# Kernel optimization log

Measured on AMD Instinct MI355X. Metric: run time of the kernel, lower is better.

Reference implementation:

```python
import jax, jax.numpy as jnp
import numpy as np

N_NODES = 100000
NUM_FEAT = 64
NUM_CLASS = 40
N_EDGES = 1600000


def setup_inputs() -> dict:
    key = jax.random.key(0)
    k1, k2, k3, k4, k5 = jax.random.split(key, 5)
    x = jax.random.normal(k1, (N_NODES, NUM_FEAT), dtype=jnp.float32)
    index = jax.random.randint(k2, (2, N_EDGES), 0, N_NODES, dtype=jnp.int64)
    # SAGEConv params: lin_l applied to aggregated neighbors (has bias),
    # lin_r applied to root features (no bias) -- PyG convention.
    s = 1.0 / np.sqrt(NUM_FEAT)
    lin_l_w = jax.random.uniform(k3, (NUM_FEAT, NUM_CLASS), dtype=jnp.float32, minval=-s, maxval=s)
    lin_l_b = jnp.zeros((NUM_CLASS,), dtype=jnp.float32)
    lin_r_w = jax.random.uniform(k4, (NUM_FEAT, NUM_CLASS), dtype=jnp.float32, minval=-s, maxval=s)
    return {"x": x, "index": index, "lin_l_w": lin_l_w, "lin_l_b": lin_l_b, "lin_r_w": lin_r_w}


def reference(x, index, lin_l_w, lin_l_b, lin_r_w):
    src, dst = index[0], index[1]
    # Mean aggregation over incoming neighbors: messages flow src -> dst.
    msg = x[src]                                        # [E, F] gather
    agg_sum = jax.ops.segment_sum(msg, dst, num_segments=N_NODES)   # [N, F]
    deg = jax.ops.segment_sum(jnp.ones((index.shape[1],), dtype=x.dtype), dst,
                              num_segments=N_NODES)     # [N]
    agg = agg_sum / jnp.maximum(deg, 1.0)[:, None]      # mean, safe for isolated nodes
    out = agg @ lin_l_w + lin_l_b + x @ lin_r_w         # [N, C]
    return jax.nn.log_softmax(out, axis=1)
```

## Files before the change

### kernel.cpp

```cpp
#include <hip/hip_runtime.h>
#include <hip/hip_fp8.h>
#include <math.h>

constexpr int NODES = 100000;
constexpr int F = 64;
constexpr int C = 40;
constexpr int NPB   = 128;
constexpr int NB    = (NODES + NPB - 1) / NPB;
constexpr int NBPAD = 1024;
constexpr int BCAP  = 2816;
constexpr int TILE  = 4096;
constexpr int NTILES = NODES / 16;
constexpr int MBLK  = (NTILES + 3) / 4;

typedef __attribute__((ext_vector_type(8))) short short8;
typedef __attribute__((ext_vector_type(4))) float floatx4;
typedef __attribute__((ext_vector_type(2))) float floatx2;

__device__ inline unsigned bf16pack2(float a, float b) {
    unsigned ua = __builtin_bit_cast(unsigned, a);
    unsigned ub = __builtin_bit_cast(unsigned, b);
    ua += 0x7FFFu + ((ua >> 16) & 1u);
    ub += 0x7FFFu + ((ub >> 16) & 1u);
    return (ua >> 16) | (ub & 0xFFFF0000u);
}
__device__ inline unsigned short bf16of(float a) {
    unsigned ua = __builtin_bit_cast(unsigned, a);
    ua += 0x7FFFu + ((ua >> 16) & 1u);
    return (unsigned short)(ua >> 16);
}
__device__ inline float bf16tof(unsigned short u) {
    return __builtin_bit_cast(float, (unsigned)u << 16);
}
__device__ inline unsigned char fp8of(float f) {
    __hip_fp8_e4m3 q(f);
    return (unsigned char)q.__x;
}
template <int K>
__device__ inline float fp8byte(unsigned d) {
    __hip_fp8_e4m3 v;
    v.__x = (__hip_fp8_storage_t)((d >> (8 * K)) & 0xFFu);
    return (float)v;
}
template <int HI>
__device__ inline floatx2 fp8pk(unsigned d) {
#if __has_builtin(__builtin_amdgcn_cvt_pk_f32_fp8)
    return __builtin_amdgcn_cvt_pk_f32_fp8((int)d, HI != 0);
#else
    floatx2 r;
    r[0] = fp8byte<HI ? 2 : 0>(d);
    r[1] = fp8byte<HI ? 3 : 1>(d);
    return r;
#endif
}

__global__ __launch_bounds__(256)
void fused_A(const float* __restrict__ x,
             const float* __restrict__ wl,
             const float* __restrict__ bl,
             const float* __restrict__ wr,
             const int* __restrict__ src, const int* __restrict__ dst,
             int* __restrict__ gcursor, int* __restrict__ bbuf, int nedges,
             unsigned char* __restrict__ y8f, unsigned short* __restrict__ z8) {
    __shared__ union {
        struct { int lhist[NB]; int lcur[NB]; } bz;
        struct { unsigned sB[10 * 64 * 4]; float sbl[40]; } mf;
    } sh;

    int t = threadIdx.x;

    if (blockIdx.x < MBLK) {
        if (t < 40) sh.mf.sbl[t] = bl[t];
        for (int s = t; s < 640; s += 256) {
            int region = s >> 6;
            int l      = s & 63;
            int ct = region >> 1, ks = region & 1;
            int col = ct * 16 + (l & 15);
            int fb  = ks * 32 + ((l >> 4) << 3);
            const float* wsrc = (col < 40) ? (wl + col) : (wr + (col - 40));
            unsigned* dstp = &sh.mf.sB[s * 4];
#pragma unroll
            for (int p = 0; p < 4; ++p) {
                float a = wsrc[(fb + 2 * p) * 40];
                float b = wsrc[(fb + 2 * p + 1) * 40];
                dstp[p] = bf16pack2(a, b);
            }
        }
        __syncthreads();

        int lane = t & 63;
        int nt = blockIdx.x * 4 + (t >> 6);
        if (nt >= NTILES) return;

        union U { unsigned u[4]; short8 v; };
        short8 bf[5][2];
#pragma unroll
        for (int ct = 0; ct < 5; ++ct)
#pragma unroll
            for (int ks = 0; ks < 2; ++ks) {
                U tmp;
                const uint4* p =
                    (const uint4*)&sh.mf.sB[((ct * 2 + ks) * 64 + lane) * 4];
                uint4 q = *p;
                tmp.u[0] = q.x; tmp.u[1] = q.y; tmp.u[2] = q.z; tmp.u[3] = q.w;
                bf[ct][ks] = tmp.v;
            }

        floatx4 acc[5];
#pragma unroll
        for (int ct = 0; ct < 5; ++ct) {
            int col = ct * 16 + (lane & 15);
            float bias = (col >= 40) ? sh.mf.sbl[col - 40] : 0.0f;
            acc[ct] = (floatx4){bias, bias, bias, bias};
        }

        int row = nt * 16 + (lane & 15);
        const float4* xp = (const float4*)(x + (size_t)row * F);
        short8 af[2];
#pragma unroll
        for (int ks = 0; ks < 2; ++ks) {
            int kb = ks * 8 + ((lane >> 4) << 1);
            float4 va = xp[kb];
            float4 vb = xp[kb + 1];
            U a;
            a.u[0] = bf16pack2(va.x, va.y);
            a.u[1] = bf16pack2(va.z, va.w);
            a.u[2] = bf16pack2(vb.x, vb.y);
            a.u[3] = bf16pack2(vb.z, vb.w);
            af[ks] = a.v;
        }

#pragma unroll
        for (int ks = 0; ks < 2; ++ks)
#pragma unroll
            for (int ct = 0; ct < 5; ++ct)
                acc[ct] = __builtin_amdgcn_mfma_f32_16x16x32_bf16(
                    af[ks], bf[ct][ks], acc[ct], 0, 0, 0);

#pragma unroll
        for (int ct = 0; ct < 5; ++ct) {
            int col = ct * 16 + (lane & 15);
#pragma unroll
            for (int r = 0; r < 4; ++r) {
                int grow = nt * 16 + ((lane >> 4) << 2) + r;
                if (col < 40) y8f[(size_t)grow * C + col]       = fp8of(acc[ct][r]);
                else          z8[(size_t)grow * C + (col - 40)] = bf16of(acc[ct][r]);
            }
        }
    } else {
        for (int i = t; i < NB; i += 256) sh.bz.lhist[i] = 0;
        __syncthreads();

        int bb = blockIdx.x - MBLK;
        int base = bb * TILE;
        int pk[16], bk[16];
#pragma unroll
        for (int u = 0; u < 16; ++u) {
            int e = base + u * 256 + t;
            bk[u] = -1;
            if (e < nedges) {
                int s = src[e], d = dst[e];
                if ((unsigned)s < (unsigned)NODES && (unsigned)d < (unsigned)NODES) {
                    bk[u] = d >> 7;
                    pk[u] = s | ((d & 127) << 17);
                    atomicAdd(&sh.bz.lhist[bk[u]], 1);
                }
            }
        }
        __syncthreads();
        for (int i = t; i < NB; i += 256) {
            int c = sh.bz.lhist[i];
            sh.bz.lcur[i] = c ? atomicAdd(&gcursor[i], c) : 0;
        }
        __syncthreads();
#pragma unroll
        for (int u = 0; u < 16; ++u) {
            if (bk[u] >= 0) {
                int p = atomicAdd(&sh.bz.lcur[bk[u]], 1);
                if (p < BCAP) bbuf[(size_t)bk[u] * BCAP + p] = pk[u];
            }
        }
    }
}

__global__ __launch_bounds__(256)
void local_sort(const int* __restrict__ bbuf, const int* __restrict__ gcount,
                int* __restrict__ sorted_src, int* __restrict__ off,
                int* __restrict__ deg) {
    __shared__ int lhist[NPB];
    __shared__ int lcur[NPB];
    __shared__ int wred[4];
    __shared__ int w0tot;

    int b = blockIdx.x;
    int t = threadIdx.x;
    int lane = t & 63, wv = t >> 6;

    int part = 0;
    for (int i = t; i < b; i += 256) part += gcount[i];
#pragma unroll
    for (int d = 1; d < 64; d <<= 1) part += __shfl_xor(part, d);
    if (lane == 0) wred[wv] = part;
    if (t < NPB) lhist[t] = 0;
    __syncthreads();
    int ebase = wred[0] + wred[1] + wred[2] + wred[3];

    int cnt = gcount[b];
    if (cnt > BCAP) cnt = BCAP;
    const int* myb = bbuf + (size_t)b * BCAP;

    for (int i = t; i < cnt; i += 256)
        atomicAdd(&lhist[myb[i] >> 17], 1);
    __syncthreads();

    int c = 0, sc = 0;
    if (t < NPB) {
        c = lhist[t];
        sc = c;
#pragma unroll
        for (int d = 1; d < 64; d <<= 1) {
            int o = __shfl_up(sc, d);
            if (lane >= d) sc += o;
        }
    }
    if (t == 63) w0tot = sc;
    __syncthreads();
    if (t >= 64 && t < NPB) sc += w0tot;
    if (t < NPB) {
        int excl = ebase + sc - c;
        lcur[t] = excl;
        int n = b * NPB + t;
        if (n < NODES) { off[n] = excl; deg[n] = c; }
    }
    __syncthreads();

    for (int i = t; i < cnt; i += 256) {
        int pk = myb[i];
        int p = atomicAdd(&lcur[pk >> 17], 1);
        sorted_src[p] = pk & 0x1FFFF;
    }
}

__device__ inline void acc8(float (&acc)[8], uint2 q) {
    floatx2 v;
    v = fp8pk<0>(q.x); acc[0] += v[0]; acc[1] += v[1];
    v = fp8pk<1>(q.x); acc[2] += v[0]; acc[3] += v[1];
    v = fp8pk<0>(q.y); acc[4] += v[0]; acc[5] += v[1];
    v = fp8pk<1>(q.y); acc[6] += v[0]; acc[7] += v[1];
}

__global__ __launch_bounds__(256)
void aggregate_v5(const unsigned char* __restrict__ y8f,
                  const unsigned short* __restrict__ z8,
                  const int* __restrict__ sorted_src,
                  const int* __restrict__ off,
                  const int* __restrict__ deg,
                  float* __restrict__ out) {
    int t = threadIdx.x;
    int lane = t & 63;
    int wv = t >> 6;
    int g = lane >> 3;
    int i = lane & 7;
    int n = blockIdx.x * 32 + wv * 8 + g;
    if (n >= NODES) return;

    bool valid = (i < 5);
    int byteoff = (valid ? i : 4) * 8;

    int base = off[n];
    int cnt  = deg[n];

    uint4 zv = make_uint4(0u, 0u, 0u, 0u);
    if (valid) zv = *(const uint4*)(z8 + (size_t)n * C + i * 8);

    float acc[8] = {0.f, 0.f, 0.f, 0.f, 0.f, 0.f, 0.f, 0.f};
    const int* sp = sorted_src + base;

    int npair = cnt >> 1;
    if (npair > 0) {
        int s0 = sp[0];
        int s1 = sp[1];
        for (int p = 0; p < npair; ++p) {
            int c0 = s0, c1 = s1;
            int nx = 2 * p + 2;
            int pi = (nx + 1 < cnt) ? nx : cnt - 2;
            s0 = sp[pi];
            s1 = sp[pi + 1];
            uint2 q0 = *(const uint2*)(y8f + (size_t)c0 * C + byteoff);
            uint2 q1 = *(const uint2*)(y8f + (size_t)c1 * C + byteoff);
            acc8(acc, q0);
            acc8(acc, q1);
        }
    }
    if (cnt & 1) {
        int c = sp[cnt - 1];
        uint2 q = *(const uint2*)(y8f + (size_t)c * C + byteoff);
        acc8(acc, q);
    }

    float inv = 1.0f / (float)(cnt > 0 ? cnt : 1);

    float o[8];
    if (valid) {
        unsigned zu[4] = {zv.x, zv.y, zv.z, zv.w};
#pragma unroll
        for (int k = 0; k < 4; ++k) {
            o[2 * k]     = bf16tof((unsigned short)(zu[k] & 0xFFFFu))
                         + acc[2 * k] * inv;
            o[2 * k + 1] = bf16tof((unsigned short)(zu[k] >> 16))
                         + acc[2 * k + 1] * inv;
        }
    } else {
#pragma unroll
        for (int k = 0; k < 8; ++k) o[k] = -1e30f;
    }

    float mv = -1e30f;
    if (valid)
#pragma unroll
        for (int k = 0; k < 8; ++k) mv = fmaxf(mv, o[k]);
#pragma unroll
    for (int m = 1; m <= 4; m <<= 1) mv = fmaxf(mv, __shfl_xor(mv, m));

    float ev = 0.0f;
    if (valid)
#pragma unroll
        for (int k = 0; k < 8; ++k) ev += __expf(o[k] - mv);
#pragma unroll
    for (int m = 1; m <= 4; m <<= 1) ev += __shfl_xor(ev, m);
    float lse = mv + __logf(ev);

    if (valid) {
        float4 o0 = make_float4(o[0] - lse, o[1] - lse, o[2] - lse, o[3] - lse);
        float4 o1 = make_float4(o[4] - lse, o[5] - lse, o[6] - lse, o[7] - lse);
        float4* op = (float4*)(out + (size_t)n * C + i * 8);
        op[0] = o0;
        op[1] = o1;
    }
}

__global__ __launch_bounds__(256)
void scatter_kernel(const float* __restrict__ x, const int* __restrict__ src,
                    const int* __restrict__ dst, float* __restrict__ aggsum,
                    float* __restrict__ deg, int nedges) {
    int lane = threadIdx.x & 63;
    int e = blockIdx.x * 4 + (threadIdx.x >> 6);
    if (e >= nedges) return;
    int s = src[e], d = dst[e];
    if ((unsigned)s >= (unsigned)NODES || (unsigned)d >= (unsigned)NODES) return;
    atomicAdd(&aggsum[(size_t)d * F + lane], x[(size_t)s * F + lane]);
    if (lane == 0) atomicAdd(&deg[d], 1.0f);
}

__global__ __launch_bounds__(256)
void meanify_kernel(float* __restrict__ aggsum, const float* __restrict__ deg) {
    int lane = threadIdx.x & 63;
    int n = blockIdx.x * 4 + (threadIdx.x >> 6);
    if (n >= NODES) return;
    aggsum[(size_t)n * F + lane] *= 1.0f / fmaxf(deg[n], 1.0f);
}

__global__ __launch_bounds__(256)
void node_kernel(const float* __restrict__ x, const float* __restrict__ aggmean,
                 const float* __restrict__ wl, const float* __restrict__ bl,
                 const float* __restrict__ wr, float* __restrict__ out) {
    __shared__ alignas(16) float sWl[F * C];
    __shared__ alignas(16) float sWr[F * C];
    __shared__ alignas(16) float sb[C];
    for (int i = threadIdx.x; i < F * C; i += 256) { sWl[i] = wl[i]; sWr[i] = wr[i]; }
    if (threadIdx.x < C) sb[threadIdx.x] = bl[threadIdx.x];
    __syncthreads();
    int n = blockIdx.x * 256 + threadIdx.x;
    if (n >= NODES) return;
    float4 acc[10];
    const float4* sb4 = (const float4*)sb;
#pragma unroll
    for (int q = 0; q < 10; ++q) acc[q] = sb4[q];
    const float4* xr  = (const float4*)(x       + (size_t)n * F);
    const float4* ar  = (const float4*)(aggmean + (size_t)n * F);
    const float4* wl4 = (const float4*)sWl;
    const float4* wr4 = (const float4*)sWr;
    for (int f4 = 0; f4 < F / 4; ++f4) {
        float4 xv = xr[f4], av = ar[f4];
        float xs[4]  = {xv.x, xv.y, xv.z, xv.w};
        float as_[4] = {av.x, av.y, av.z, av.w};
#pragma unroll
        for (int jj = 0; jj < 4; ++jj) {
            int f = f4 * 4 + jj;
#pragma unroll
            for (int q = 0; q < 10; ++q) {
                float4 wlv = wl4[f * 10 + q], wrv = wr4[f * 10 + q];
                acc[q].x = fmaf(as_[jj], wlv.x, fmaf(xs[jj], wrv.x, acc[q].x));
                acc[q].y = fmaf(as_[jj], wlv.y, fmaf(xs[jj], wrv.y, acc[q].y));
                acc[q].z = fmaf(as_[jj], wlv.z, fmaf(xs[jj], wrv.z, acc[q].z));
                acc[q].w = fmaf(as_[jj], wlv.w, fmaf(xs[jj], wrv.w, acc[q].w));
            }
        }
    }
    float m = -1e30f;
#pragma unroll
    for (int q = 0; q < 10; ++q)
        m = fmaxf(m, fmaxf(fmaxf(acc[q].x, acc[q].y), fmaxf(acc[q].z, acc[q].w)));
    float ssum = 0.0f;
#pragma unroll
    for (int q = 0; q < 10; ++q)
        ssum += __expf(acc[q].x - m) + __expf(acc[q].y - m) +
                __expf(acc[q].z - m) + __expf(acc[q].w - m);
    float lse = m + __logf(ssum);
    float4* op = (float4*)(out + (size_t)n * C);
#pragma unroll
    for (int q = 0; q < 10; ++q) {
        float4 v;
        v.x = acc[q].x - lse; v.y = acc[q].y - lse;
        v.z = acc[q].z - lse; v.w = acc[q].w - lse;
        op[q] = v;
    }
}

extern "C" void kernel_launch(void* const* d_in, const int* in_sizes, int n_in,
                              void* d_out, int out_size, void* d_ws, size_t ws_size,
                              hipStream_t stream) {
    const float* x     = (const float*)d_in[0];
    const int*   index = (const int*)d_in[1];
    const float* wl    = (const float*)d_in[2];
    const float* bl    = (const float*)d_in[3];
    const float* wr    = (const float*)d_in[4];
    float* out = (float*)d_out;

    int nedges = in_sizes[1] / 2;
    const int* src = index;
    const int* dst = index + nedges;

    size_t need = (size_t)NODES * C * 3
                + ((size_t)NB * BCAP + (size_t)nedges + 2 * (size_t)NODES + NBPAD) * 4;

    if (ws_size >= need) {
        unsigned short* z8 = (unsigned short*)d_ws;
        unsigned char* y8f = (unsigned char*)(z8 + (size_t)NODES * C);
        int* bbuf       = (int*)(y8f + (size_t)NODES * C);
        int* sorted_src = bbuf + (size_t)NB * BCAP;
        int* off        = sorted_src + nedges;
        int* deg        = off + NODES;
        int* gcursor    = deg + NODES;

        hipMemsetAsync(gcursor, 0, NBPAD * sizeof(int), stream);

        int bblocks = (nedges + TILE - 1) / TILE;
        fused_A<<<MBLK + bblocks, 256, 0, stream>>>(
            x, wl, bl, wr, src, dst, gcursor, bbuf, nedges, y8f, z8);
        local_sort<<<NB, 256, 0, stream>>>(bbuf, gcursor, sorted_src, off, deg);
        aggregate_v5<<<(NODES + 31) / 32, 256, 0, stream>>>(
            y8f, z8, sorted_src, off, deg, out);
    } else {
        float* aggsum = (float*)d_ws;
        float* deg    = aggsum + (size_t)NODES * F;
        hipMemsetAsync(d_ws, 0,
                       ((size_t)NODES * F + NODES) * sizeof(float), stream);
        scatter_kernel<<<(nedges + 3) / 4, 256, 0, stream>>>(
            x, src, dst, aggsum, deg, nedges);
        meanify_kernel<<<(NODES + 3) / 4, 256, 0, stream>>>(aggsum, deg);
        node_kernel<<<(NODES + 255) / 256, 256, 0, stream>>>(
            x, aggsum, wl, bl, wr, out);
    }
}
```

Before: 150.8 us.

## Fuse per-bucket local sort into aggregation kernel using LDS-resident sorted sources

```diff
diff --git a/kernel.cpp b/kernel.cpp
--- a/kernel.cpp
+++ b/kernel.cpp
@@ -183,64 +183,6 @@
     }
 }
 
-__global__ __launch_bounds__(256)
-void local_sort(const int* __restrict__ bbuf, const int* __restrict__ gcount,
-                int* __restrict__ sorted_src, int* __restrict__ off,
-                int* __restrict__ deg) {
-    __shared__ int lhist[NPB];
-    __shared__ int lcur[NPB];
-    __shared__ int wred[4];
-    __shared__ int w0tot;
-
-    int b = blockIdx.x;
-    int t = threadIdx.x;
-    int lane = t & 63, wv = t >> 6;
-
-    int part = 0;
-    for (int i = t; i < b; i += 256) part += gcount[i];
-#pragma unroll
-    for (int d = 1; d < 64; d <<= 1) part += __shfl_xor(part, d);
-    if (lane == 0) wred[wv] = part;
-    if (t < NPB) lhist[t] = 0;
-    __syncthreads();
-    int ebase = wred[0] + wred[1] + wred[2] + wred[3];
-
-    int cnt = gcount[b];
-    if (cnt > BCAP) cnt = BCAP;
-    const int* myb = bbuf + (size_t)b * BCAP;
-
-    for (int i = t; i < cnt; i += 256)
-        atomicAdd(&lhist[myb[i] >> 17], 1);
-    __syncthreads();
-
-    int c = 0, sc = 0;
-    if (t < NPB) {
-        c = lhist[t];
-        sc = c;
-#pragma unroll
-        for (int d = 1; d < 64; d <<= 1) {
-            int o = __shfl_up(sc, d);
-            if (lane >= d) sc += o;
-        }
-    }
-    if (t == 63) w0tot = sc;
-    __syncthreads();
-    if (t >= 64 && t < NPB) sc += w0tot;
-    if (t < NPB) {
-        int excl = ebase + sc - c;
-        lcur[t] = excl;
-        int n = b * NPB + t;
-        if (n < NODES) { off[n] = excl; deg[n] = c; }
-    }
-    __syncthreads();
-
-    for (int i = t; i < cnt; i += 256) {
-        int pk = myb[i];
-        int p = atomicAdd(&lcur[pk >> 17], 1);
-        sorted_src[p] = pk & 0x1FFFF;
-    }
-}
-
 __device__ inline void acc8(float (&acc)[8], uint2 q) {
     floatx2 v;
     v = fp8pk<0>(q.x); acc[0] += v[0]; acc[1] += v[1];
@@ -250,92 +192,133 @@
 }
 
 __global__ __launch_bounds__(256)
-void aggregate_v5(const unsigned char* __restrict__ y8f,
-                  const unsigned short* __restrict__ z8,
-                  const int* __restrict__ sorted_src,
-                  const int* __restrict__ off,
-                  const int* __restrict__ deg,
-                  float* __restrict__ out) {
+void sort_aggregate(const unsigned char* __restrict__ y8f,
+                    const unsigned short* __restrict__ z8,
+                    const int* __restrict__ bbuf,
+                    const int* __restrict__ gcount,
+                    float* __restrict__ out) {
+    __shared__ int lhist[NPB];
+    __shared__ int lcur[NPB];
+    __shared__ int slds[BCAP];
+    __shared__ int w0tot;
+
+    int b = blockIdx.x;
     int t = threadIdx.x;
     int lane = t & 63;
-    int wv = t >> 6;
-    int g = lane >> 3;
-    int i = lane & 7;
-    int n = blockIdx.x * 32 + wv * 8 + g;
-    if (n >= NODES) return;
-
+
+    if (t < NPB) lhist[t] = 0;
+    __syncthreads();
+
+    int cnt = gcount[b];
+    if (cnt > BCAP) cnt = BCAP;
+    const int* myb = bbuf + (size_t)b * BCAP;
+
+    for (int i = t; i < cnt; i += 256)
+        atomicAdd(&lhist[myb[i] >> 17], 1);
+    __syncthreads();
+
+    int c = 0, sc = 0;
+    if (t < NPB) {
+        c = lhist[t];
+        sc = c;
+#pragma unroll
+        for (int d = 1; d < 64; d <<= 1) {
+            int o = __shfl_up(sc, d);
+            if (lane >= d) sc += o;
+        }
+    }
+    if (t == 63) w0tot = sc;
+    __syncthreads();
+    if (t >= 64 && t < NPB) sc += w0tot;
+    if (t < NPB) lcur[t] = sc - c;
+    __syncthreads();
+
+    for (int i = t; i < cnt; i += 256) {
+        int pk = myb[i];
+        int p = atomicAdd(&lcur[pk >> 17], 1);
+        slds[p] = pk & 0x1FFFF;
+    }
+    __syncthreads();
+
+    int gid = t >> 3;
+    int i = t & 7;
     bool valid = (i < 5);
     int byteoff = (valid ? i : 4) * 8;
 
-    int base = off[n];
-    int cnt  = deg[n];
-
-    uint4 zv = make_uint4(0u, 0u, 0u, 0u);
-    if (valid) zv = *(const uint4*)(z8 + (size_t)n * C + i * 8);
-
-    float acc[8] = {0.f, 0.f, 0.f, 0.f, 0.f, 0.f, 0.f, 0.f};
-    const int* sp = sorted_src + base;
-
-    int npair = cnt >> 1;
-    if (npair > 0) {
-        int s0 = sp[0];
-        int s1 = sp[1];
-        for (int p = 0; p < npair; ++p) {
-            int c0 = s0, c1 = s1;
-            int nx = 2 * p + 2;
-            int pi = (nx + 1 < cnt) ? nx : cnt - 2;
-            s0 = sp[pi];
-            s1 = sp[pi + 1];
-            uint2 q0 = *(const uint2*)(y8f + (size_t)c0 * C + byteoff);
-            uint2 q1 = *(const uint2*)(y8f + (size_t)c1 * C + byteoff);
-            acc8(acc, q0);
-            acc8(acc, q1);
-        }
-    }
-    if (cnt & 1) {
-        int c = sp[cnt - 1];
-        uint2 q = *(const uint2*)(y8f + (size_t)c * C + byteoff);
-        acc8(acc, q);
-    }
-
-    float inv = 1.0f / (float)(cnt > 0 ? cnt : 1);
-
-    float o[8];
-    if (valid) {
-        unsigned zu[4] = {zv.x, zv.y, zv.z, zv.w};
-#pragma unroll
-        for (int k = 0; k < 4; ++k) {
-            o[2 * k]     = bf16tof((unsigned short)(zu[k] & 0xFFFFu))
-                         + acc[2 * k] * inv;
-            o[2 * k + 1] = bf16tof((unsigned short)(zu[k] >> 16))
-                         + acc[2 * k + 1] * inv;
-        }
-    } else {
-#pragma unroll
-        for (int k = 0; k < 8; ++k) o[k] = -1e30f;
-    }
-
-    float mv = -1e30f;
-    if (valid)
-#pragma unroll
-        for (int k = 0; k < 8; ++k) mv = fmaxf(mv, o[k]);
-#pragma unroll
-    for (int m = 1; m <= 4; m <<= 1) mv = fmaxf(mv, __shfl_xor(mv, m));
-
-    float ev = 0.0f;
-    if (valid)
-#pragma unroll
-        for (int k = 0; k < 8; ++k) ev += __expf(o[k] - mv);
-#pragma unroll
-    for (int m = 1; m <= 4; m <<= 1) ev += __shfl_xor(ev, m);
-    float lse = mv + __logf(ev);
-
-    if (valid) {
-        float4 o0 = make_float4(o[0] - lse, o[1] - lse, o[2] - lse, o[3] - lse);
-        float4 o1 = make_float4(o[4] - lse, o[5] - lse, o[6] - lse, o[7] - lse);
-        float4* op = (float4*)(out + (size_t)n * C + i * 8);
-        op[0] = o0;
-        op[1] = o1;
+    for (int j = 0; j < 4; ++j) {
+        int nd = gid * 4 + j;
+        int n = b * NPB + nd;
+        if (n >= NODES) break;
+
+        int dg = lhist[nd];
+        const int* sp = slds + (lcur[nd] - dg);
+
+        uint4 zv = make_uint4(0u, 0u, 0u, 0u);
+        if (valid) zv = *(const uint4*)(z8 + (size_t)n * C + i * 8);
+
+        float acc[8] = {0.f, 0.f, 0.f, 0.f, 0.f, 0.f, 0.f, 0.f};
+
+        int npair = dg >> 1;
+        if (npair > 0) {
+            int s0 = sp[0];
+            int s1 = sp[1];
+            for (int p = 0; p < npair; ++p) {
+                int c0 = s0, c1 = s1;
+                int nx = 2 * p + 2;
+                int pi = (nx + 1 < dg) ? nx : dg - 2;
+                s0 = sp[pi];
+                s1 = sp[pi + 1];
+                uint2 q0 = *(const uint2*)(y8f + (size_t)c0 * C + byteoff);
+                uint2 q1 = *(const uint2*)(y8f + (size_t)c1 * C + byteoff);
+                acc8(acc, q0);
+                acc8(acc, q1);
+            }
+        }
+        if (dg & 1) {
+            int cl = sp[dg - 1];
+            uint2 q = *(const uint2*)(y8f + (size_t)cl * C + byteoff);
+            acc8(acc, q);
+        }
+
+        float inv = 1.0f / (float)(dg > 0 ? dg : 1);
+
+        float o[8];
+        if (valid) {
+            unsigned zu[4] = {zv.x, zv.y, zv.z, zv.w};
+#pragma unroll
+            for (int k = 0; k < 4; ++k) {
+                o[2 * k]     = bf16tof((unsigned short)(zu[k] & 0xFFFFu))
+                             + acc[2 * k] * inv;
+                o[2 * k + 1] = bf16tof((unsigned short)(zu[k] >> 16))
+                             + acc[2 * k + 1] * inv;
+            }
+        } else {
+#pragma unroll
+            for (int k = 0; k < 8; ++k) o[k] = -1e30f;
+        }
+
+        float mv = -1e30f;
+        if (valid)
+#pragma unroll
+            for (int k = 0; k < 8; ++k) mv = fmaxf(mv, o[k]);
+#pragma unroll
+        for (int m = 1; m <= 4; m <<= 1) mv = fmaxf(mv, __shfl_xor(mv, m));
+
+        float ev = 0.0f;
+        if (valid)
+#pragma unroll
+            for (int k = 0; k < 8; ++k) ev += __expf(o[k] - mv);
+#pragma unroll
+        for (int m = 1; m <= 4; m <<= 1) ev += __shfl_xor(ev, m);
+        float lse = mv + __logf(ev);
+
+        if (valid) {
+            float4 o0 = make_float4(o[0] - lse, o[1] - lse, o[2] - lse, o[3] - lse);
+            float4 o1 = make_float4(o[4] - lse, o[5] - lse, o[6] - lse, o[7] - lse);
+            float4* op = (float4*)(out + (size_t)n * C + i * 8);
+            op[0] = o0;
+            op[1] = o1;
+        }
     }
 }
 
@@ -432,25 +415,21 @@
     const int* dst = index + nedges;
 
     size_t need = (size_t)NODES * C * 3
-                + ((size_t)NB * BCAP + (size_t)nedges + 2 * (size_t)NODES + NBPAD) * 4;
+                + ((size_t)NB * BCAP + NBPAD) * 4;
 
     if (ws_size >= need) {
         unsigned short* z8 = (unsigned short*)d_ws;
         unsigned char* y8f = (unsigned char*)(z8 + (size_t)NODES * C);
         int* bbuf       = (int*)(y8f + (size_t)NODES * C);
-        int* sorted_src = bbuf + (size_t)NB * BCAP;
-        int* off        = sorted_src + nedges;
-        int* deg        = off + NODES;
-        int* gcursor    = deg + NODES;
+        int* gcursor    = bbuf + (size_t)NB * BCAP;
 
         hipMemsetAsync(gcursor, 0, NBPAD * sizeof(int), stream);
 
         int bblocks = (nedges + TILE - 1) / TILE;
         fused_A<<<MBLK + bblocks, 256, 0, stream>>>(
             x, wl, bl, wr, src, dst, gcursor, bbuf, nedges, y8f, z8);
-        local_sort<<<NB, 256, 0, stream>>>(bbuf, gcursor, sorted_src, off, deg);
-        aggregate_v5<<<(NODES + 31) / 32, 256, 0, stream>>>(
-            y8f, z8, sorted_src, off, deg, out);
+        sort_aggregate<<<NB, 256, 0, stream>>>(
+            y8f, z8, bbuf, gcursor, out);
     } else {
         float* aggsum = (float*)d_ws;
         float* deg    = aggsum + (size_t)NODES * F;
```

Result: faster. 139.8 us (-7.3%).
